# Kernel optimization log

Measured on AMD Instinct MI355X. Metric: run time of the kernel, lower is better.

The kernel has to match this reference:

```python
import jax, jax.numpy as jnp
import numpy as np

EPS = 1e-5  # torch BatchNorm default eps
SLOPE = 0.2  # LeakyReLU negative slope


def bn_apply(h, p):
    # p: (4, C) stacked [gamma, beta, running_mean, running_var]; h channel-last
    g, b, m, v = p[0], p[1], p[2], p[3]
    return (h - m) * (g * jax.lax.rsqrt(v + EPS)) + b


def graph_feature(x, k):
    # x: (B, N, C) -> (B, N, k, 2C) = concat(neighbor - center, center)
    inner = jnp.einsum('bnc,bmc->bnm', x, x)
    sq = jnp.sum(x * x, axis=-1)
    # negative squared pairwise distance (B, N, N)
    pd = 2.0 * inner - sq[:, :, None] - sq[:, None, :]
    idx = jax.lax.top_k(pd, k)[1]  # (B, N, k)
    nbr = jax.vmap(lambda xb, ib: xb[ib])(x, idx)  # (B, N, k, C) gather
    ctr = jnp.broadcast_to(x[:, :, None, :], nbr.shape)
    return jnp.concatenate([nbr - ctr, ctr], axis=-1)


def edge_block(h, w, bnp, k):
    # h: (B, N, C); w: (O, 2C) 1x1 conv weight; returns (B, N, O) after max over k
    f = graph_feature(h, k)
    z = jnp.einsum('bnkc,oc->bnko', f, w)
    z = jax.nn.leaky_relu(bn_apply(z, bnp), SLOPE)
    return jnp.max(z, axis=2)


def setup_inputs() -> dict:
    key = jax.random.key(0)
    ks = jax.random.split(key, 10)
    B, N, K = 16, 1024, 20
    emb, ncls = 1024, 40

    def bnp(c):
        return jnp.stack([jnp.ones(c), jnp.zeros(c), jnp.zeros(c), jnp.ones(c)])

    s = 0.05
    return {
        'x': jax.random.normal(ks[0], (B, 3, N), dtype=jnp.float32),
        'w1': jax.random.normal(ks[1], (64, 6), dtype=jnp.float32) * s,
        'bn1': bnp(64),
        'w2': jax.random.normal(ks[2], (64, 128), dtype=jnp.float32) * s,
        'bn2': bnp(64),
        'w3': jax.random.normal(ks[3], (128, 128), dtype=jnp.float32) * s,
        'bn3': bnp(128),
        'w4': jax.random.normal(ks[4], (256, 256), dtype=jnp.float32) * s,
        'bn4': bnp(256),
        'w5': jax.random.normal(ks[5], (emb, 512), dtype=jnp.float32) * s,
        'bn5': bnp(emb),
        'wl1': jax.random.normal(ks[6], (512, 2 * emb), dtype=jnp.float32) * s,
        'bn6': bnp(512),
        'wl2': jax.random.normal(ks[7], (256, 512), dtype=jnp.float32) * s,
        'bn7': bnp(256),
        'wl3': jax.random.normal(ks[8], (ncls, 256), dtype=jnp.float32) * s,
        'bl3': jax.random.normal(ks[9], (ncls,), dtype=jnp.float32) * s,
        'k': K,
    }


def reference(x, w1, bn1, w2, bn2, w3, bn3, w4, bn4, w5, bn5,
              wl1, bn6, wl2, bn7, wl3, bl3, k):
    # x: (B, 3, N) -> logits (B, num_classes); eval-mode BN, dropout = identity
    h0 = jnp.transpose(x, (0, 2, 1))  # (B, N, 3)
    x1 = edge_block(h0, w1, bn1, k)   # (B, N, 64)
    x2 = edge_block(x1, w2, bn2, k)   # (B, N, 64)
    x3 = edge_block(x2, w3, bn3, k)   # (B, N, 128)
    x4 = edge_block(x3, w4, bn4, k)   # (B, N, 256)
    h = jnp.concatenate([x1, x2, x3, x4], axis=-1)  # (B, N, 512)
    h = jax.nn.leaky_relu(bn_apply(jnp.einsum('bnc,oc->bno', h, w5), bn5), SLOPE)
    p = jnp.concatenate([jnp.max(h, axis=1), jnp.mean(h, axis=1)], axis=-1)  # (B, 2*emb)
    h = jax.nn.leaky_relu(bn_apply(p @ wl1.T, bn6), SLOPE)
    h = jax.nn.leaky_relu(bn_apply(h @ wl2.T, bn7), SLOPE)
    return h @ wl3.T + bl3
```

## Files before the change

### kernel.cpp

```cpp
#include <hip/hip_runtime.h>

#define BB 16
#define NN 1024
#define KNN 20
#define BNEPS 1e-5f

typedef __attribute__((ext_vector_type(8))) short short8;
typedef __attribute__((ext_vector_type(4))) float f32x4;

__device__ __forceinline__ float4 ld4(const float* p){ return *(const float4*)p; }
__device__ __forceinline__ void fma4(float4& a, float s, float4 w){
  a.x = fmaf(s, w.x, a.x); a.y = fmaf(s, w.y, a.y);
  a.z = fmaf(s, w.z, a.z); a.w = fmaf(s, w.w, a.w);
}
__device__ __forceinline__ void max4(float4& a, float4 v){
  a.x = fmaxf(a.x, v.x); a.y = fmaxf(a.y, v.y);
  a.z = fmaxf(a.z, v.z); a.w = fmaxf(a.w, v.w);
}
__device__ __forceinline__ unsigned short f2bf(float f){
  unsigned int u = __float_as_uint(f);
  u = (u + 0x7FFF + ((u >> 16) & 1)) >> 16;
  return (unsigned short)u;
}
__device__ __forceinline__ float bf2f(unsigned short u){
  return __uint_as_float(((unsigned int)u) << 16);
}
__device__ __forceinline__ f32x4 mfma16(short8 a, short8 b, f32x4 c){
  return __builtin_amdgcn_mfma_f32_16x16x32_bf16(a, b, c, 0, 0, 0);
}

__device__ __forceinline__ void top3_build(const float* rp, int kmr,
                                           float& a0, float& a1, float& a2,
                                           int& i0, int& i1, int& i2){
  a0 = -1e30f; a1 = -1e30f; a2 = -1e30f; i0 = 0; i1 = 0; i2 = 0;
#pragma unroll
  for (int r = 0; r < 4; r++){
    float4 t = ld4(rp + r*4);
    float tv[4] = {t.x, t.y, t.z, t.w};
#pragma unroll
    for (int q = 0; q < 4; q++){
      int e = r*4 + q;
      float v = ((kmr >> e) & 1) ? -1e30f : tv[q];
      bool b0 = v > a0, b1 = v > a1, b2 = v > a2;
      a2 = b1 ? a1 : (b2 ? v : a2); i2 = b1 ? i1 : (b2 ? e : i2);
      a1 = b0 ? a0 : (b1 ? v : a1); i1 = b0 ? i0 : (b1 ? e : i1);
      a0 = b0 ? v  : a0;            i0 = b0 ? e : i0;
    }
  }
}

__device__ __forceinline__ void topk_body(int bid, int tidx,
                                          const float* __restrict__ pd, int* __restrict__ idxOut){
  int w = tidx >> 6, lane = tidx & 63;
  const int xcd = bid & 7, j = bid >> 3;
  const int b = xcd + ((j >> 7) << 3);
  const int local = j & 127;
  int bn0 = (b*128 + local)*8 + w*2;
  const float* row0 = pd + (size_t)bn0*NN + lane*16;
  const float* row1 = row0 + NN;

  float c0v[2], c1v[2], c2v[2];
  int   c0i[2], c1i[2], c2i[2];
  int   km[2] = {0, 0};
  top3_build(row0, 0, c0v[0], c1v[0], c2v[0], c0i[0], c1i[0], c2i[0]);
  top3_build(row1, 0, c0v[1], c1v[1], c2v[1], c0i[1], c1i[1], c2i[1]);

  int* out0 = idxOut + (size_t)bn0*KNN;
  int* out1 = out0 + KNN;
  for (int it = 0; it < KNN; it++){
    float g0 = c0v[0], g1 = c0v[1];
#pragma unroll
    for (int s = 1; s < 64; s <<= 1){
      g0 = fmaxf(g0, __shfl_xor(g0, s));
      g1 = fmaxf(g1, __shfl_xor(g1, s));
    }
    int o0 = __ffsll(__ballot(c0v[0] == g0)) - 1;
    int o1 = __ffsll(__ballot(c0v[1] == g1)) - 1;
    bool u0 = (lane == o0), u1 = (lane == o1);
    if (u0) out0[it] = lane*16 + c0i[0];
    if (u1) out1[it] = lane*16 + c0i[1];
    km[0] |= u0 ? (1 << c0i[0]) : 0;
    km[1] |= u1 ? (1 << c0i[1]) : 0;
    c0v[0] = u0 ? c1v[0] : c0v[0];  c0i[0] = u0 ? c1i[0] : c0i[0];
    c1v[0] = u0 ? c2v[0] : c1v[0];  c1i[0] = u0 ? c2i[0] : c1i[0];
    c2v[0] = u0 ? -1e30f : c2v[0];
    c0v[1] = u1 ? c1v[1] : c0v[1];  c0i[1] = u1 ? c1i[1] : c0i[1];
    c1v[1] = u1 ? c2v[1] : c1v[1];  c1i[1] = u1 ? c2i[1] : c1i[1];
    c2v[1] = u1 ? -1e30f : c2v[1];
    if (it < KNN-1){
      bool rp0 = (c0v[0] == -1e30f) && (km[0] != 0xFFFF);
      bool rp1 = (c0v[1] == -1e30f) && (km[1] != 0xFFFF);
      if (__ballot(rp0 || rp1)){
        if (rp0) top3_build(row0, km[0], c0v[0], c1v[0], c2v[0], c0i[0], c1i[0], c2i[0]);
        if (rp1) top3_build(row1, km[1], c0v[1], c1v[1], c2v[1], c0i[1], c1i[1], c2i[1]);
      }
    }
  }
}

__device__ __forceinline__ void prep_w_dev(int i, const float* w, const float* bnp,
                                           float* wlT, float* dT, float* bias, int Cin, int Cpad, int Cout){
  if (i >= Cpad*Cout) return;
  int c = i / Cout, o = i - c*Cout;
  float s = bnp[o] * rsqrtf(bnp[3*Cout+o] + BNEPS);
  float wl = (c < Cin) ? w[(size_t)o*2*Cin + c] : 0.f;
  float wr = (c < Cin) ? w[(size_t)o*2*Cin + Cin + c] : 0.f;
  wlT[i] = wl * s;
  dT[i]  = (wr - wl) * s;
  if (c == 0) bias[o] = bnp[Cout+o] - bnp[2*Cout+o]*s;
}
__device__ __forceinline__ void prep_wbf_dev(int i, const float* w, const float* bnp,
                                             unsigned short* wlB, unsigned short* dB, float* bias,
                                             int Cin, int Cout){
  if (i >= Cin*Cout) return;
  int o = i / Cin, c = i - o*Cin;
  float s = bnp[o] * rsqrtf(bnp[3*Cout+o] + BNEPS);
  float wl = w[(size_t)o*2*Cin + c] * s;
  float wr = w[(size_t)o*2*Cin + Cin + c] * s;
  wlB[i] = f2bf(wl);
  dB[i]  = f2bf(wr - wl);
  if (c == 0) bias[o] = bnp[Cout+o] - bnp[2*Cout+o]*s;
}

__global__ __launch_bounds__(256) void k_init(const float* __restrict__ x, float* __restrict__ xt,
                                              unsigned short* __restrict__ hlo, float* __restrict__ sq,
                                              const float* __restrict__ w1, const float* __restrict__ bn1,
                                              const float* __restrict__ w2, const float* __restrict__ bn2,
                                              const float* __restrict__ w3, const float* __restrict__ bn3,
                                              const float* __restrict__ w4, const float* __restrict__ bn4,
                                              const float* __restrict__ w5, const float* __restrict__ bn5,
                                              float* __restrict__ wlT1, float* __restrict__ dT1, float* __restrict__ bias1,
                                              unsigned short* __restrict__ wlB2, unsigned short* __restrict__ dB2, float* __restrict__ bias2,
                                              unsigned short* __restrict__ wlB3, unsigned short* __restrict__ dB3, float* __restrict__ bias3,
                                              unsigned short* __restrict__ wlB4, unsigned short* __restrict__ dB4, float* __restrict__ bias4,
                                              unsigned short* __restrict__ w5b, float* __restrict__ b5){
  const int t = threadIdx.x;
  if (blockIdx.x < 64){
    int i = blockIdx.x*256 + t;
    int b = i >> 10, n = i & 1023;
    const float* xb = x + (size_t)b*3*NN;
    float4 v;
    v.x = xb[0*NN+n]; v.y = xb[1*NN+n]; v.z = xb[2*NN+n]; v.w = 0.f;
    ((float4*)xt)[i] = v;
    unsigned short hx = f2bf(v.x), hy = f2bf(v.y), hz = f2bf(v.z);
    float rx = v.x - bf2f(hx), ry = v.y - bf2f(hy), rz = v.z - bf2f(hz);
    unsigned short lx = f2bf(rx), ly = f2bf(ry), lz = f2bf(rz);
    float ex = bf2f(hx)+bf2f(lx), ey = bf2f(hy)+bf2f(ly), ez = bf2f(hz)+bf2f(lz);
    sq[i] = ex*ex + ey*ey + ez*ez;
    ushort4 h4 = {hx, hy, hz, 0};
    ushort4 l4 = {lx, ly, lz, 0};
    ushort4 z4 = {0, 0, 0, 0};
    unsigned short* pa = hlo + (size_t)i*512 + 256;
    unsigned short* pb = hlo + (size_t)i*512 + 288;
    *(ushort4*)(pa+0) = h4; *(ushort4*)(pa+4) = l4; *(ushort4*)(pa+8) = h4;
    *(ushort4*)(pb+0) = h4; *(ushort4*)(pb+4) = h4; *(ushort4*)(pb+8) = l4;
#pragma unroll
    for (int s = 12; s < 32; s += 4){ *(ushort4*)(pa+s) = z4; *(ushort4*)(pb+s) = z4; }
    return;
  }
  int bid = blockIdx.x - 64;
  if (bid < 1){
    prep_w_dev(t, w1, bn1, wlT1, dT1, bias1, 3, 4, 64);
  } else if (bid < 17){
    prep_wbf_dev((bid-1)*256 + t, w2, bn2, wlB2, dB2, bias2, 64, 64);
  } else if (bid < 49){
    prep_wbf_dev((bid-17)*256 + t, w3, bn3, wlB3, dB3, bias3, 64, 128);
  } else if (bid < 177){
    prep_wbf_dev((bid-49)*256 + t, w4, bn4, wlB4, dB4, bias4, 128, 256);
  } else {
    int i = (bid-177)*256 + t;
    int o = i >> 9, c = i & 511;
    float s = bn5[o] * rsqrtf(bn5[3*1024+o] + BNEPS);
    w5b[i] = f2bf(w5[(size_t)o*512 + c] * s);
    if (c == 0) b5[o] = bn5[1024+o] - bn5[2*1024+o]*s;
  }
}

template<int CC>
__global__ __launch_bounds__(256) void k_pdm(const unsigned short* __restrict__ hbi,
                                             const unsigned short* __restrict__ hlo,
                                             const float* __restrict__ sq,
                                             float* __restrict__ pd){
  __shared__ char sm[20480];
  char* As = sm; char* Bs = sm + 10240;
  const int tid = threadIdx.x, lane = tid & 63, w = tid >> 6;
  const int l15 = lane & 15, quad = lane >> 4;
  const int bid = blockIdx.x;
  const int xcd = bid & 7, j = bid >> 3;
  const int b = xcd + ((j >> 6) << 3);
  const int rt = (j >> 3) & 7, ct = j & 7;
  const size_t ar0 = (size_t)b*NN + rt*128;
  const size_t br0 = (size_t)b*NN + ct*128;
  const int colb = ct*128;

  f32x4 acc[2][8];
  f32x4 zero = {0.f,0.f,0.f,0.f};
#pragma unroll
  for (int i = 0; i < 2; i++)
#pragma unroll
    for (int j2 = 0; j2 < 8; j2++) acc[i][j2] = zero;

  for (int k0 = 0; k0 < 3*CC; k0 += 32){
    int seg = k0 / CC, off = k0 - seg*CC;
    const unsigned short* Ap = (seg == 1) ? hlo : hbi;
    const unsigned short* Bp = (seg == 2) ? hlo : hbi;
#pragma unroll
    for (int i = 0; i < 2; i++){
      int e = tid + i*256;
      int r = e >> 2, sg = e & 3;
      *(float4*)(As + r*80 + sg*16) = *(const float4*)(Ap + (ar0+r)*512 + off + sg*8);
      *(float4*)(Bs + r*80 + sg*16) = *(const float4*)(Bp + (br0+r)*512 + off + sg*8);
    }
    __syncthreads();
    short8 af0 = *(short8*)(As + (w*32 + l15)*80 + quad*16);
    short8 af1 = *(short8*)(As + (w*32 + 16 + l15)*80 + quad*16);
#pragma unroll
    for (int ns = 0; ns < 8; ns++){
      short8 bf = *(short8*)(Bs + (ns*16 + l15)*80 + quad*16);
      acc[0][ns] = mfma16(af0, bf, acc[0][ns]);
      acc[1][ns] = mfma16(af1, bf, acc[1][ns]);
    }
    __syncthreads();
  }

  float* L = (float*)sm;
#pragma unroll
  for (int p = 0; p < 4; p++){
    const int ms = p >> 1, nh = p & 1;
    __syncthreads();
#pragma unroll
    for (int ns = 0; ns < 4; ns++){
      f32x4 a = acc[ms][nh*4 + ns];
      float sqv = sq[br0 + (nh*4+ns)*16 + l15];
#pragma unroll
      for (int r = 0; r < 4; r++)
        L[(w*16 + quad*4 + r)*68 + ns*16 + l15] = 2.f*a[r] - sqv;
    }
    __syncthreads();
#pragma unroll
    for (int k = 0; k < 4; k++){
      int e = tid + k*256;
      int lr = e >> 4, c4 = (e & 15)*4;
      int grow = (int)ar0 + (lr >> 4)*32 + ms*16 + (lr & 15);
      *(float4*)(pd + (size_t)grow*NN + colb + nh*64 + c4) = *(float4*)(L + lr*68 + c4);
    }
  }
}

__global__ __launch_bounds__(256) void k_pdm1(const unsigned short* __restrict__ hlo,
                                              const float* __restrict__ sq,
                                              float* __restrict__ pd){
  __shared__ char sm[20480];
  char* As = sm; char* Bs = sm + 10240;
  const int tid = threadIdx.x, lane = tid & 63, w = tid >> 6;
  const int l15 = lane & 15, quad = lane >> 4;
  const int bid = blockIdx.x;
  const int xcd = bid & 7, j = bid >> 3;
  const int b = xcd + ((j >> 6) << 3);
  const int rt = (j >> 3) & 7, ct = j & 7;
  const size_t ar0 = (size_t)b*NN + rt*128;
  const size_t br0 = (size_t)b*NN + ct*128;
  const int colb = ct*128;

#pragma unroll
  for (int i = 0; i < 2; i++){
    int e = tid + i*256;
    int r = e >> 2, sg = e & 3;
    *(float4*)(As + r*80 + sg*16) = *(const float4*)(hlo + (ar0+r)*512 + 256 + sg*8);
    *(float4*)(Bs + r*80 + sg*16) = *(const float4*)(hlo + (br0+r)*512 + 288 + sg*8);
  }
  __syncthreads();

  f32x4 acc[2][8];
  f32x4 zero = {0.f,0.f,0.f,0.f};
#pragma unroll
  for (int i = 0; i < 2; i++)
#pragma unroll
    for (int j2 = 0; j2 < 8; j2++) acc[i][j2] = zero;

  short8 af0 = *(short8*)(As + (w*32 + l15)*80 + quad*16);
  short8 af1 = *(short8*)(As + (w*32 + 16 + l15)*80 + quad*16);
#pragma unroll
  for (int ns = 0; ns < 8; ns++){
    short8 bf = *(short8*)(Bs + (ns*16 + l15)*80 + quad*16);
    acc[0][ns] = mfma16(af0, bf, acc[0][ns]);
    acc[1][ns] = mfma16(af1, bf, acc[1][ns]);
  }

  float* L = (float*)sm;
#pragma unroll
  for (int p = 0; p < 4; p++){
    const int ms = p >> 1, nh = p & 1;
    __syncthreads();
#pragma unroll
    for (int ns = 0; ns < 4; ns++){
      f32x4 a = acc[ms][nh*4 + ns];
      float sqv = sq[br0 + (nh*4+ns)*16 + l15];
#pragma unroll
      for (int r = 0; r < 4; r++)
        L[(w*16 + quad*4 + r)*68 + ns*16 + l15] = 2.f*a[r] - sqv;
    }
    __syncthreads();
#pragma unroll
    for (int k = 0; k < 4; k++){
      int e = tid + k*256;
      int lr = e >> 4, c4 = (e & 15)*4;
      int grow = (int)ar0 + (lr >> 4)*32 + ms*16 + (lr & 15);
      *(float4*)(pd + (size_t)grow*NN + colb + nh*64 + c4) = *(float4*)(L + lr*68 + c4);
    }
  }
}

template<int K, int NY>
__global__ __launch_bounds__(256) void k_tkuv(const float* __restrict__ pd, int* __restrict__ idxOut,
                                              const unsigned short* __restrict__ hbi,
                                              const unsigned short* __restrict__ wB,
                                              float* __restrict__ Z, int ldz){
  __shared__ char sm[20480];
  if (blockIdx.x < 2048){
    topk_body(blockIdx.x, threadIdx.x, pd, idxOut);
    return;
  }
  char* As = sm; char* Bs = sm + 10240;
  const int tid = threadIdx.x, lane = tid & 63, w = tid >> 6;
  const int l15 = lane & 15, quad = lane >> 4;
  const int jj = blockIdx.x - 2048;
  const int bx = jj & 127;
  const int t = ((bx & 7) << 3) | ((bx >> 3) & 7) | (bx & 64);
  const int n0 = (jj >> 7)*128, r0 = t*128;

  f32x4 acc[2][8];
  f32x4 zero = {0.f,0.f,0.f,0.f};
#pragma unroll
  for (int i = 0; i < 2; i++)
#pragma unroll
    for (int j = 0; j < 8; j++) acc[i][j] = zero;

  for (int k0 = 0; k0 < K; k0 += 32){
#pragma unroll
    for (int i = 0; i < 2; i++){
      int e = tid + i*256;
      int r = e >> 2, sg = e & 3;
      *(float4*)(As + r*80 + sg*16) = *(const float4*)(hbi + ((size_t)(r0+r))*512 + k0 + sg*8);
      *(float4*)(Bs + r*80 + sg*16) = *(const float4*)(wB  + ((size_t)(n0+r))*K   + k0 + sg*8);
    }
    __syncthreads();
    short8 af0 = *(short8*)(As + (w*32 + l15)*80 + quad*16);
    short8 af1 = *(short8*)(As + (w*32 + 16 + l15)*80 + quad*16);
#pragma unroll
    for (int ns = 0; ns < 8; ns++){
      short8 bf = *(short8*)(Bs + (ns*16 + l15)*80 + quad*16);
      acc[0][ns] = mfma16(af0, bf, acc[0][ns]);
      acc[1][ns] = mfma16(af1, bf, acc[1][ns]);
    }
    __syncthreads();
  }

#pragma unroll
  for (int ms = 0; ms < 2; ms++){
#pragma unroll
    for (int ns = 0; ns < 8; ns++){
      f32x4 a = acc[ms][ns];
      int row = r0 + w*32 + ms*16 + quad*4;
      int col = n0 + ns*16 + l15;
#pragma unroll
      for (int r = 0; r < 4; r++)
        Z[(size_t)(row+r)*ldz + col] = a[r];
    }
  }
}

__global__ __launch_bounds__(256) void k_tkuv1(const float* __restrict__ pd, int* __restrict__ idxOut,
                                               const float* __restrict__ xt,
                                               const float* __restrict__ wlT, const float* __restrict__ dT,
                                               float* __restrict__ Z){
  if (blockIdx.x < 2048){
    topk_body(blockIdx.x, threadIdx.x, pd, idxOut);
    return;
  }
  const int bid = blockIdx.x - 2048;
  const int pb = ((bid >> 10) << 10) | ((bid & 7) << 7) | ((bid >> 3) & 127);
  int t = pb*256 + threadIdx.x;
  int n = t >> 5, q = t & 31;
  float4 xv = ld4(xt + (size_t)n*4);
  const float* wp = (q < 16) ? (wlT + q*4) : (dT + (q-16)*4);
  float4 a = make_float4(0.f,0.f,0.f,0.f);
  fma4(a, xv.x, ld4(wp + 0*64));
  fma4(a, xv.y, ld4(wp + 1*64));
  fma4(a, xv.z, ld4(wp + 2*64));
  fma4(a, xv.w, ld4(wp + 3*64));
  *(float4*)(Z + (size_t)n*128 + q*4) = a;
}

template<int COUT, int P, bool WLO>
__global__ __launch_bounds__(256) void k_gmax(const float* __restrict__ Z,
                                              const float* __restrict__ bias,
                                              const int* __restrict__ knn_idx,
                                              unsigned short* __restrict__ hbo,
                                              unsigned short* __restrict__ hloo,
                                              float* __restrict__ sqo){
  constexpr int QPP = COUT/4;
  constexpr int BPB = 1024/P;
  constexpr int SHF = (P == 16) ? 6 : (P == 8) ? 7 : 8;
  __shared__ int idxS[P*KNN];
  const int tid = threadIdx.x;
  const int bid = blockIdx.x;
  const int pb = ((bid >> (SHF+3)) << (SHF+3)) | ((bid & 7) << SHF) | ((bid >> 3) & (BPB-1));
  const int p0 = pb * P;
  for (int t = tid; t < P*KNN; t += 256) idxS[t] = knn_idx[(size_t)p0*KNN + t];
  __syncthreads();

  const int p = tid / QPP, q = tid - p*QPP;
  const int base = p0 & ~1023;
  const int ldz = 2*COUT;
  const float* Zq = Z + q*4;

  float4 m = make_float4(-1e30f,-1e30f,-1e30f,-1e30f);
#pragma unroll
  for (int j = 0; j < KNN; j++){
    int mr = idxS[p*KNN + j];
    max4(m, ld4(Zq + (size_t)(base + mr)*ldz));
  }
  float4 ctr = ld4(Z + (size_t)(p0+p)*ldz + COUT + q*4);
  float4 bs  = ld4(bias + q*4);
  float4 y;
  y.x = m.x + ctr.x + bs.x; y.x = fmaxf(y.x, 0.2f*y.x);
  y.y = m.y + ctr.y + bs.y; y.y = fmaxf(y.y, 0.2f*y.y);
  y.z = m.z + ctr.z + bs.z; y.z = fmaxf(y.z, 0.2f*y.z);
  y.w = m.w + ctr.w + bs.w; y.w = fmaxf(y.w, 0.2f*y.w);

  size_t pi = (size_t)(p0 + p);
  ushort4 hv; hv.x = f2bf(y.x); hv.y = f2bf(y.y); hv.z = f2bf(y.z); hv.w = f2bf(y.w);
  *(ushort4*)(hbo + pi*512 + q*4) = hv;
  if (WLO){
    ushort4 lv;
    lv.x = f2bf(y.x - bf2f(hv.x)); lv.y = f2bf(y.y - bf2f(hv.y));
    lv.z = f2bf(y.z - bf2f(hv.z)); lv.w = f2bf(y.w - bf2f(hv.w));
    *(ushort4*)(hloo + pi*512 + q*4) = lv;
    float ex = bf2f(hv.x)+bf2f(lv.x), ey = bf2f(hv.y)+bf2f(lv.y);
    float ez = bf2f(hv.z)+bf2f(lv.z), ew = bf2f(hv.w)+bf2f(lv.w);
    float s4 = ex*ex + ey*ey + ez*ez + ew*ew;
#pragma unroll
    for (int sh = 1; sh < QPP; sh <<= 1) s4 += __shfl_xor(s4, sh);
    if (q == 0) sqo[pi] = s4;
  }
}

__global__ __launch_bounds__(256) void k_conv5m(const unsigned short* __restrict__ hb,
                                                const unsigned short* __restrict__ w5b,
                                                const float* __restrict__ b5,
                                                float* __restrict__ pmax, float* __restrict__ psum){
  __shared__ char sm[20480 + 4096];
  char* As = sm; char* Bs = sm + 10240;
  float* red = (float*)(sm + 20480);
  const int tid = threadIdx.x, lane = tid & 63, w = tid >> 6;
  const int l15 = lane & 15, quad = lane >> 4;
  const int n0 = blockIdx.y*128, r0 = blockIdx.x*128;

  f32x4 acc[2][8];
  f32x4 zero = {0.f,0.f,0.f,0.f};
#pragma unroll
  for (int i = 0; i < 2; i++)
#pragma unroll
    for (int j = 0; j < 8; j++) acc[i][j] = zero;

  for (int k0 = 0; k0 < 512; k0 += 32){
#pragma unroll
    for (int i = 0; i < 2; i++){
      int e = tid + i*256;
      int r = e >> 2, sg = e & 3;
      *(float4*)(As + r*80 + sg*16) = *(const float4*)(hb  + ((size_t)(r0+r))*512 + k0 + sg*8);
      *(float4*)(Bs + r*80 + sg*16) = *(const float4*)(w5b + ((size_t)(n0+r))*512 + k0 + sg*8);
    }
    __syncthreads();
    short8 af0 = *(short8*)(As + (w*32 + l15)*80 + quad*16);
    short8 af1 = *(short8*)(As + (w*32 + 16 + l15)*80 + quad*16);
#pragma unroll
    for (int ns = 0; ns < 8; ns++){
      short8 bf = *(short8*)(Bs + (ns*16 + l15)*80 + quad*16);
      acc[0][ns] = mfma16(af0, bf, acc[0][ns]);
      acc[1][ns] = mfma16(af1, bf, acc[1][ns]);
    }
    __syncthreads();
  }

#pragma unroll
  for (int ns = 0; ns < 8; ns++){
    float bv = b5[n0 + ns*16 + l15];
    float mx = -1e30f, sum = 0.f;
#pragma unroll
    for (int ms = 0; ms < 2; ms++){
      float* a = (float*)&acc[ms][ns];
#pragma unroll
      for (int r = 0; r < 4; r++){
        float v = a[r] + bv; v = fmaxf(v, 0.2f*v);
        mx = fmaxf(mx, v); sum += v;
      }
    }
    for (int s = 16; s < 64; s <<= 1){
      mx = fmaxf(mx, __shfl_xor(mx, s));
      sum += __shfl_xor(sum, s);
    }
    if (quad == 0){ red[(w*8 + ns)*16 + l15] = mx; red[512 + (w*8 + ns)*16 + l15] = sum; }
  }
  __syncthreads();
  if (tid < 128){
    int ns = tid >> 4, ci = tid & 15;
    float mx = -1e30f, sum = 0.f;
#pragma unroll
    for (int w2 = 0; w2 < 4; w2++){
      mx = fmaxf(mx, red[(w2*8 + ns)*16 + ci]);
      sum += red[512 + (w2*8 + ns)*16 + ci];
    }
    pmax[(size_t)blockIdx.x*1024 + n0 + tid] = mx;
    psum[(size_t)blockIdx.x*1024 + n0 + tid] = sum;
  }
}

__global__ __launch_bounds__(256) void k_fc1(const float* __restrict__ pmax, const float* __restrict__ psum,
                                             const float* __restrict__ wl1, const float* __restrict__ bn6,
                                             float* __restrict__ h1){
  __shared__ float pS[2048];
  const int b = blockIdx.y, t = threadIdx.x;
  for (int f = t; f < 512; f += 256){
    float4 r;
    if (f < 256){
      r = ld4(pmax + (size_t)(b*8)*1024 + f*4);
#pragma unroll
      for (int ch = 1; ch < 8; ch++) max4(r, ld4(pmax + (size_t)(b*8+ch)*1024 + f*4));
    } else {
      int o = (f-256)*4;
      r = ld4(psum + (size_t)(b*8)*1024 + o);
#pragma unroll
      for (int ch = 1; ch < 8; ch++){
        float4 s = ld4(psum + (size_t)(b*8+ch)*1024 + o);
        r.x += s.x; r.y += s.y; r.z += s.z; r.w += s.w;
      }
      r.x *= (1.f/1024.f); r.y *= (1.f/1024.f); r.z *= (1.f/1024.f); r.w *= (1.f/1024.f);
    }
    ((float4*)pS)[f] = r;
  }
  __syncthreads();
  const int ol = t >> 4, ch = t & 15;
  const int o = blockIdx.x*16 + ol;
  const float* wr = wl1 + (size_t)o*2048;
  float acc = 0.f;
#pragma unroll
  for (int j = 0; j < 32; j++){
    int c = ch*4 + j*64;
    float4 wv = ld4(wr + c);
    acc += pS[c]*wv.x + pS[c+1]*wv.y + pS[c+2]*wv.z + pS[c+3]*wv.w;
  }
#pragma unroll
  for (int s = 1; s < 16; s <<= 1) acc += __shfl_xor(acc, s);
  if (ch == 0){
    float s = bn6[o] * rsqrtf(bn6[3*512+o] + BNEPS);
    float y = (acc - bn6[2*512+o])*s + bn6[512+o];
    h1[(size_t)b*512 + o] = fmaxf(y, 0.2f*y);
  }
}

__global__ __launch_bounds__(256) void k_fc2(const float* __restrict__ h1,
                                             const float* __restrict__ wl2, const float* __restrict__ bn7,
                                             float* __restrict__ h2){
  __shared__ float hS[512];
  const int b = blockIdx.y, t = threadIdx.x;
  if (t < 128) ((float4*)hS)[t] = ((const float4*)(h1 + (size_t)b*512))[t];
  __syncthreads();
  const int ol = t >> 4, ch = t & 15;
  const int o = blockIdx.x*16 + ol;
  const float* wr = wl2 + (size_t)o*512;
  float acc = 0.f;
#pragma unroll
  for (int j = 0; j < 8; j++){
    int c = ch*4 + j*64;
    float4 wv = ld4(wr + c);
    acc += hS[c]*wv.x + hS[c+1]*wv.y + hS[c+2]*wv.z + hS[c+3]*wv.w;
  }
#pragma unroll
  for (int s = 1; s < 16; s <<= 1) acc += __shfl_xor(acc, s);
  if (ch == 0){
    float s = bn7[o] * rsqrtf(bn7[3*256+o] + BNEPS);
    float y = (acc - bn7[2*256+o])*s + bn7[256+o];
    h2[(size_t)b*256 + o] = fmaxf(y, 0.2f*y);
  }
}

__global__ __launch_bounds__(64) void k_fc3(const float* __restrict__ h2,
                                            const float* __restrict__ wl3, const float* __restrict__ bl3,
                                            float* __restrict__ out){
  const int o = blockIdx.x, b = blockIdx.y, lane = threadIdx.x;
  float4 wv = ld4(wl3 + (size_t)o*256 + lane*4);
  float4 hv = ld4(h2 + (size_t)b*256 + lane*4);
  float acc = hv.x*wv.x + hv.y*wv.y + hv.z*wv.z + hv.w*wv.w;
#pragma unroll
  for (int s = 1; s < 64; s <<= 1) acc += __shfl_xor(acc, s);
  if (lane == 0) out[(size_t)b*40 + o] = acc + bl3[o];
}

extern "C" void kernel_launch(void* const* d_in, const int* in_sizes, int n_in,
                              void* d_out, int out_size, void* d_ws, size_t ws_size,
                              hipStream_t stream) {
  (void)in_sizes; (void)n_in; (void)out_size; (void)ws_size;
  const float* x   = (const float*)d_in[0];
  const float* w1  = (const float*)d_in[1];
  const float* bn1 = (const float*)d_in[2];
  const float* w2  = (const float*)d_in[3];
  const float* bn2 = (const float*)d_in[4];
  const float* w3  = (const float*)d_in[5];
  const float* bn3 = (const float*)d_in[6];
  const float* w4  = (const float*)d_in[7];
  const float* bn4 = (const float*)d_in[8];
  const float* w5  = (const float*)d_in[9];
  const float* bn5 = (const float*)d_in[10];
  const float* wl1 = (const float*)d_in[11];
  const float* bn6 = (const float*)d_in[12];
  const float* wl2 = (const float*)d_in[13];
  const float* bn7 = (const float*)d_in[14];
  const float* wl3 = (const float*)d_in[15];
  const float* bl3 = (const float*)d_in[16];
  float* out = (float*)d_out;

  float* ws    = (float*)d_ws;
  float* xt    = ws;
  float* sqb   = xt + 65536;
  int*   idxb  = (int*)(sqb + 16384);
  float* pd    = (float*)(idxb + 327680);
  unsigned short* hlo = (unsigned short*)(pd + 16777216);
  float* wlT1  = (float*)(hlo + 8388608);
  float* dT1   = wlT1 + 256;
  float* bias1 = dT1 + 256;
  float* bias2 = bias1 + 64;
  float* bias3 = bias2 + 64;
  float* bias4 = bias3 + 128;
  float* b5    = bias4 + 256;
  float* pmax  = b5 + 1024;
  float* psum  = pmax + 131072;
  float* pool  = psum + 131072;
  float* h1b   = pool + 32768;
  float* h2b   = h1b + 8192;
  unsigned short* hb   = (unsigned short*)(h2b + 4096);
  unsigned short* wlB2 = hb + (size_t)16384*512;
  unsigned short* dB2  = wlB2 + 4096;
  unsigned short* wlB3 = dB2 + 4096;
  unsigned short* dB3  = wlB3 + 8192;
  unsigned short* wlB4 = dB3 + 8192;
  unsigned short* dB4  = wlB4 + 32768;
  unsigned short* w5b  = dB4 + 32768;
  float* Z = (float*)(w5b + 524288);

  k_init<<<2289, 256, 0, stream>>>(x, xt, hlo, sqb,
                                   w1, bn1, w2, bn2, w3, bn3, w4, bn4, w5, bn5,
                                   wlT1, dT1, bias1, wlB2, dB2, bias2,
                                   wlB3, dB3, bias3, wlB4, dB4, bias4, w5b, b5);

  k_pdm1<<<1024, 256, 0, stream>>>(hlo, sqb, pd);
  k_tkuv1<<<4096, 256, 0, stream>>>(pd, idxb, xt, wlT1, dT1, Z);
  k_gmax<64,16,true><<<1024, 256, 0, stream>>>(Z, bias1, idxb, hb, hlo, sqb);

  k_pdm<64><<<1024, 256, 0, stream>>>(hb, hlo, sqb, pd);
  k_tkuv<64,1><<<2048+128, 256, 0, stream>>>(pd, idxb, hb, wlB2, Z, 128);
  k_gmax<64,16,true><<<1024, 256, 0, stream>>>(Z, bias2, idxb, hb + 64, hlo + 64, sqb);

  k_pdm<64><<<1024, 256, 0, stream>>>(hb + 64, hlo + 64, sqb, pd);
  k_tkuv<64,2><<<2048+256, 256, 0, stream>>>(pd, idxb, hb + 64, wlB3, Z, 256);
  k_gmax<128,8,true><<<2048, 256, 0, stream>>>(Z, bias3, idxb, hb + 128, hlo + 128, sqb);

  k_pdm<128><<<1024, 256, 0, stream>>>(hb + 128, hlo + 128, sqb, pd);
  k_tkuv<128,4><<<2048+512, 256, 0, stream>>>(pd, idxb, hb + 128, wlB4, Z, 512);
  k_gmax<256,4,false><<<4096, 256, 0, stream>>>(Z, bias4, idxb, hb + 256, nullptr, nullptr);

  k_conv5m<<<dim3(128,8), 256, 0, stream>>>(hb, w5b, b5, pmax, psum);
  k_fc1<<<dim3(32,16), 256, 0, stream>>>(pmax, psum, wl1, bn6, h1b);
  k_fc2<<<dim3(16,16), 256, 0, stream>>>(h1b, wl2, bn7, h2b);
  k_fc3<<<dim3(40,16), 64, 0, stream>>>(h2b, wl3, bl3, out);
}
```

Baseline: 403.4 us.

## Split edge-conv stages by batch halves and fuse across layers to overlap

Each edge-conv layer's pairwise-distance, top-k, projection and gather-max stages now run on two halves of the batch. They are fused into skewed combined kernels (D1/D2/D3), so one half's stage runs alongside the other half's different stage in the same launch. The intent is to mix compute-bound GEMM blocks with memory- and latency-bound top-k and gather blocks, shrinking tail effects and idle gaps between dependent launches. The Z buffer uses a fixed row stride of 512 so both halves can share it. The cost is more complex indexing, extra kernel variants, and possible cache contention between the mixed workloads.

Measured after the change: 439.6 us. 9.0% more time.

```diff
diff --git a/kernel.cpp b/kernel.cpp
--- a/kernel.cpp
+++ b/kernel.cpp
@@ -4,6 +4,7 @@
 #define NN 1024
 #define KNN 20
 #define BNEPS 1e-5f
+#define LDZ 512
 
 typedef __attribute__((ext_vector_type(8))) short short8;
 typedef __attribute__((ext_vector_type(4))) float f32x4;
@@ -49,12 +50,9 @@
   }
 }
 
-__device__ __forceinline__ void topk_body(int bid, int tidx,
+__device__ __forceinline__ void topk_rows(int b, int local, int tidx,
                                           const float* __restrict__ pd, int* __restrict__ idxOut){
   int w = tidx >> 6, lane = tidx & 63;
-  const int xcd = bid & 7, j = bid >> 3;
-  const int b = xcd + ((j >> 7) << 3);
-  const int local = j & 127;
   int bn0 = (b*128 + local)*8 + w*2;
   const float* row0 = pd + (size_t)bn0*NN + lane*16;
   const float* row1 = row0 + NN;
@@ -96,6 +94,13 @@
       }
     }
   }
+}
+__device__ __forceinline__ void topk_full(int bid, int tidx, const float* pd, int* idxOut){
+  const int xcd = bid & 7, j = bid >> 3;
+  topk_rows(xcd + ((j >> 7) << 3), j & 127, tidx, pd, idxOut);
+}
+__device__ __forceinline__ void topk_half(int bid, int b0, int tidx, const float* pd, int* idxOut){
+  topk_rows((bid & 7) + b0, (bid >> 3) & 127, tidx, pd, idxOut);
 }
 
 __device__ __forceinline__ void prep_w_dev(int i, const float* w, const float* bnp,
@@ -177,17 +182,16 @@
 }
 
 template<int CC>
-__global__ __launch_bounds__(256) void k_pdm(const unsigned short* __restrict__ hbi,
-                                             const unsigned short* __restrict__ hlo,
-                                             const float* __restrict__ sq,
-                                             float* __restrict__ pd){
-  __shared__ char sm[20480];
+__device__ __forceinline__ void pdm_body(char* sm, int bid, int b0,
+                                         const unsigned short* __restrict__ hbi,
+                                         const unsigned short* __restrict__ hlo,
+                                         const float* __restrict__ sq,
+                                         float* __restrict__ pd){
   char* As = sm; char* Bs = sm + 10240;
   const int tid = threadIdx.x, lane = tid & 63, w = tid >> 6;
   const int l15 = lane & 15, quad = lane >> 4;
-  const int bid = blockIdx.x;
-  const int xcd = bid & 7, j = bid >> 3;
-  const int b = xcd + ((j >> 6) << 3);
+  const int b = (bid & 7) + b0;
+  const int j = bid >> 3;
   const int rt = (j >> 3) & 7, ct = j & 7;
   const size_t ar0 = (size_t)b*NN + rt*128;
   const size_t br0 = (size_t)b*NN + ct*128;
@@ -311,23 +315,17 @@
   }
 }
 
-template<int K, int NY>
-__global__ __launch_bounds__(256) void k_tkuv(const float* __restrict__ pd, int* __restrict__ idxOut,
-                                              const unsigned short* __restrict__ hbi,
-                                              const unsigned short* __restrict__ wB,
-                                              float* __restrict__ Z, int ldz){
-  __shared__ char sm[20480];
-  if (blockIdx.x < 2048){
-    topk_body(blockIdx.x, threadIdx.x, pd, idxOut);
-    return;
-  }
+template<int K>
+__device__ __forceinline__ void uv_body(char* sm, int bid, int b0,
+                                        const unsigned short* __restrict__ hbi,
+                                        const unsigned short* __restrict__ wB,
+                                        float* __restrict__ Z){
   char* As = sm; char* Bs = sm + 10240;
   const int tid = threadIdx.x, lane = tid & 63, w = tid >> 6;
   const int l15 = lane & 15, quad = lane >> 4;
-  const int jj = blockIdx.x - 2048;
-  const int bx = jj & 127;
-  const int t = ((bx & 7) << 3) | ((bx >> 3) & 7) | (bx & 64);
-  const int n0 = (jj >> 7)*128, r0 = t*128;
+  const int bx = bid & 63, ny = bid >> 6;
+  const int t8 = ((bx & 7) << 3) | ((bx >> 3) & 7);
+  const int n0 = ny*128, r0 = (t8 + b0*8)*128;
 
   f32x4 acc[2][8];
   f32x4 zero = {0.f,0.f,0.f,0.f};
@@ -365,8 +363,60 @@
       int col = n0 + ns*16 + l15;
 #pragma unroll
       for (int r = 0; r < 4; r++)
-        Z[(size_t)(row+r)*ldz + col] = a[r];
-    }
+        Z[(size_t)(row+r)*LDZ + col] = a[r];
+    }
+  }
+}
+
+template<int COUT, int P, bool WLO>
+__device__ __forceinline__ void gmax_body(char* smraw, int bid, int b0,
+                                          const float* __restrict__ Z,
+                                          const float* __restrict__ bias,
+                                          const int* __restrict__ knn_idx,
+                                          unsigned short* __restrict__ hbo,
+                                          unsigned short* __restrict__ hloo,
+                                          float* __restrict__ sqo){
+  constexpr int QPP = COUT/4;
+  constexpr int BPB = 1024/P;
+  int* idxS = (int*)smraw;
+  const int tid = threadIdx.x;
+  const int pb = ((bid & 7) + b0)*BPB + ((bid >> 3) & (BPB-1));
+  const int p0 = pb * P;
+  for (int t = tid; t < P*KNN; t += 256) idxS[t] = knn_idx[(size_t)p0*KNN + t];
+  __syncthreads();
+
+  const int p = tid / QPP, q = tid - p*QPP;
+  const int base = p0 & ~1023;
+  const float* Zq = Z + q*4;
+
+  float4 m = make_float4(-1e30f,-1e30f,-1e30f,-1e30f);
+#pragma unroll
+  for (int j = 0; j < KNN; j++){
+    int mr = idxS[p*KNN + j];
+    max4(m, ld4(Zq + (size_t)(base + mr)*LDZ));
+  }
+  float4 ctr = ld4(Z + (size_t)(p0+p)*LDZ + COUT + q*4);
+  float4 bs  = ld4(bias + q*4);
+  float4 y;
+  y.x = m.x + ctr.x + bs.x; y.x = fmaxf(y.x, 0.2f*y.x);
+  y.y = m.y + ctr.y + bs.y; y.y = fmaxf(y.y, 0.2f*y.y);
+  y.z = m.z + ctr.z + bs.z; y.z = fmaxf(y.z, 0.2f*y.z);
+  y.w = m.w + ctr.w + bs.w; y.w = fmaxf(y.w, 0.2f*y.w);
+
+  size_t pi = (size_t)(p0 + p);
+  ushort4 hv; hv.x = f2bf(y.x); hv.y = f2bf(y.y); hv.z = f2bf(y.z); hv.w = f2bf(y.w);
+  *(ushort4*)(hbo + pi*512 + q*4) = hv;
+  if (WLO){
+    ushort4 lv;
+    lv.x = f2bf(y.x - bf2f(hv.x)); lv.y = f2bf(y.y - bf2f(hv.y));
+    lv.z = f2bf(y.z - bf2f(hv.z)); lv.w = f2bf(y.w - bf2f(hv.w));
+    *(ushort4*)(hloo + pi*512 + q*4) = lv;
+    float ex = bf2f(hv.x)+bf2f(lv.x), ey = bf2f(hv.y)+bf2f(lv.y);
+    float ez = bf2f(hv.z)+bf2f(lv.z), ew = bf2f(hv.w)+bf2f(lv.w);
+    float s4 = ex*ex + ey*ey + ez*ez + ew*ew;
+#pragma unroll
+    for (int sh = 1; sh < QPP; sh <<= 1) s4 += __shfl_xor(s4, sh);
+    if (q == 0) sqo[pi] = s4;
   }
 }
 
@@ -375,7 +425,7 @@
                                                const float* __restrict__ wlT, const float* __restrict__ dT,
                                                float* __restrict__ Z){
   if (blockIdx.x < 2048){
-    topk_body(blockIdx.x, threadIdx.x, pd, idxOut);
+    topk_full(blockIdx.x, threadIdx.x, pd, idxOut);
     return;
   }
   const int bid = blockIdx.x - 2048;
@@ -389,61 +439,55 @@
   fma4(a, xv.y, ld4(wp + 1*64));
   fma4(a, xv.z, ld4(wp + 2*64));
   fma4(a, xv.w, ld4(wp + 3*64));
-  *(float4*)(Z + (size_t)n*128 + q*4) = a;
+  *(float4*)(Z + (size_t)n*LDZ + q*4) = a;
 }
 
 template<int COUT, int P, bool WLO>
-__global__ __launch_bounds__(256) void k_gmax(const float* __restrict__ Z,
-                                              const float* __restrict__ bias,
-                                              const int* __restrict__ knn_idx,
-                                              unsigned short* __restrict__ hbo,
-                                              unsigned short* __restrict__ hloo,
-                                              float* __restrict__ sqo){
-  constexpr int QPP = COUT/4;
-  constexpr int BPB = 1024/P;
-  constexpr int SHF = (P == 16) ? 6 : (P == 8) ? 7 : 8;
-  __shared__ int idxS[P*KNN];
-  const int tid = threadIdx.x;
-  const int bid = blockIdx.x;
-  const int pb = ((bid >> (SHF+3)) << (SHF+3)) | ((bid & 7) << SHF) | ((bid >> 3) & (BPB-1));
-  const int p0 = pb * P;
-  for (int t = tid; t < P*KNN; t += 256) idxS[t] = knn_idx[(size_t)p0*KNN + t];
-  __syncthreads();
-
-  const int p = tid / QPP, q = tid - p*QPP;
-  const int base = p0 & ~1023;
-  const int ldz = 2*COUT;
-  const float* Zq = Z + q*4;
-
-  float4 m = make_float4(-1e30f,-1e30f,-1e30f,-1e30f);
-#pragma unroll
-  for (int j = 0; j < KNN; j++){
-    int mr = idxS[p*KNN + j];
-    max4(m, ld4(Zq + (size_t)(base + mr)*ldz));
-  }
-  float4 ctr = ld4(Z + (size_t)(p0+p)*ldz + COUT + q*4);
-  float4 bs  = ld4(bias + q*4);
-  float4 y;
-  y.x = m.x + ctr.x + bs.x; y.x = fmaxf(y.x, 0.2f*y.x);
-  y.y = m.y + ctr.y + bs.y; y.y = fmaxf(y.y, 0.2f*y.y);
-  y.z = m.z + ctr.z + bs.z; y.z = fmaxf(y.z, 0.2f*y.z);
-  y.w = m.w + ctr.w + bs.w; y.w = fmaxf(y.w, 0.2f*y.w);
-
-  size_t pi = (size_t)(p0 + p);
-  ushort4 hv; hv.x = f2bf(y.x); hv.y = f2bf(y.y); hv.z = f2bf(y.z); hv.w = f2bf(y.w);
-  *(ushort4*)(hbo + pi*512 + q*4) = hv;
-  if (WLO){
-    ushort4 lv;
-    lv.x = f2bf(y.x - bf2f(hv.x)); lv.y = f2bf(y.y - bf2f(hv.y));
-    lv.z = f2bf(y.z - bf2f(hv.z)); lv.w = f2bf(y.w - bf2f(hv.w));
-    *(ushort4*)(hloo + pi*512 + q*4) = lv;
-    float ex = bf2f(hv.x)+bf2f(lv.x), ey = bf2f(hv.y)+bf2f(lv.y);
-    float ez = bf2f(hv.z)+bf2f(lv.z), ew = bf2f(hv.w)+bf2f(lv.w);
-    float s4 = ex*ex + ey*ey + ez*ez + ew*ew;
-#pragma unroll
-    for (int sh = 1; sh < QPP; sh <<= 1) s4 += __shfl_xor(s4, sh);
-    if (q == 0) sqo[pi] = s4;
-  }
+__global__ __launch_bounds__(256) void k_gmaxH(int b0, const float* __restrict__ Z,
+                                               const float* __restrict__ bias, const int* __restrict__ idx,
+                                               unsigned short* __restrict__ hbo,
+                                               unsigned short* __restrict__ hloo, float* __restrict__ sqo){
+  __shared__ char sm[20480];
+  gmax_body<COUT,P,WLO>(sm, blockIdx.x, b0, Z, bias, idx, hbo, hloo, sqo);
+}
+
+template<int CC, int COUT, int P, bool WLO>
+__global__ __launch_bounds__(256) void k_D1(const unsigned short* __restrict__ hbi,
+                                            const unsigned short* __restrict__ hloi,
+                                            const float* __restrict__ sq, float* __restrict__ pd,
+                                            const float* __restrict__ Z, const float* __restrict__ bias,
+                                            const int* __restrict__ idx,
+                                            unsigned short* __restrict__ hbo,
+                                            unsigned short* __restrict__ hloo, float* __restrict__ sqo){
+  __shared__ char sm[20480];
+  if (blockIdx.x < 512) pdm_body<CC>(sm, blockIdx.x, 0, hbi, hloi, sq, pd);
+  else gmax_body<COUT,P,WLO>(sm, blockIdx.x - 512, 8, Z, bias, idx, hbo, hloo, sqo);
+}
+
+template<int CC, int K, int NY>
+__global__ __launch_bounds__(256) void k_D2(const unsigned short* __restrict__ hbi,
+                                            const unsigned short* __restrict__ hloi,
+                                            const float* __restrict__ sq, float* __restrict__ pd,
+                                            const unsigned short* __restrict__ wB,
+                                            float* __restrict__ Z, int* __restrict__ idxOut){
+  __shared__ char sm[20480];
+  if (blockIdx.x < 512) pdm_body<CC>(sm, blockIdx.x, 8, hbi, hloi, sq, pd);
+  else if (blockIdx.x < 512 + NY*64) uv_body<K>(sm, blockIdx.x - 512, 0, hbi, wB, Z);
+  else topk_half(blockIdx.x - (512 + NY*64), 0, threadIdx.x, pd, idxOut);
+}
+
+template<int K, int NY, int COUT, int P, bool WLO>
+__global__ __launch_bounds__(256) void k_D3(const float* __restrict__ pd, int* __restrict__ idxOut,
+                                            const unsigned short* __restrict__ hbi,
+                                            const unsigned short* __restrict__ wB, float* __restrict__ Z,
+                                            const float* __restrict__ bias,
+                                            unsigned short* __restrict__ hbo,
+                                            unsigned short* __restrict__ hloo, float* __restrict__ sqo){
+  __shared__ char sm[20480];
+  constexpr int GH = 8 * (1024/P);
+  if (blockIdx.x < GH) gmax_body<COUT,P,WLO>(sm, blockIdx.x, 0, Z, bias, idxOut, hbo, hloo, sqo);
+  else if (blockIdx.x < GH + NY*64) uv_body<K>(sm, blockIdx.x - GH, 8, hbi, wB, Z);
+  else topk_half(blockIdx.x - (GH + NY*64), 8, threadIdx.x, pd, idxOut);
 }
 
 __global__ __launch_bounds__(256) void k_conv5m(const unsigned short* __restrict__ hb,
@@ -656,19 +700,20 @@
 
   k_pdm1<<<1024, 256, 0, stream>>>(hlo, sqb, pd);
   k_tkuv1<<<4096, 256, 0, stream>>>(pd, idxb, xt, wlT1, dT1, Z);
-  k_gmax<64,16,true><<<1024, 256, 0, stream>>>(Z, bias1, idxb, hb, hlo, sqb);
-
-  k_pdm<64><<<1024, 256, 0, stream>>>(hb, hlo, sqb, pd);
-  k_tkuv<64,1><<<2048+128, 256, 0, stream>>>(pd, idxb, hb, wlB2, Z, 128);
-  k_gmax<64,16,true><<<1024, 256, 0, stream>>>(Z, bias2, idxb, hb + 64, hlo + 64, sqb);
-
-  k_pdm<64><<<1024, 256, 0, stream>>>(hb + 64, hlo + 64, sqb, pd);
-  k_tkuv<64,2><<<2048+256, 256, 0, stream>>>(pd, idxb, hb + 64, wlB3, Z, 256);
-  k_gmax<128,8,true><<<2048, 256, 0, stream>>>(Z, bias3, idxb, hb + 128, hlo + 128, sqb);
-
-  k_pdm<128><<<1024, 256, 0, stream>>>(hb + 128, hlo + 128, sqb, pd);
-  k_tkuv<128,4><<<2048+512, 256, 0, stream>>>(pd, idxb, hb + 128, wlB4, Z, 512);
-  k_gmax<256,4,false><<<4096, 256, 0, stream>>>(Z, bias4, idxb, hb + 256, nullptr, nullptr);
+  k_gmaxH<64,16,true><<<512, 256, 0, stream>>>(0, Z, bias1, idxb, hb, hlo, sqb);
+
+  k_D1<64,64,16,true><<<1024, 256, 0, stream>>>(hb, hlo, sqb, pd, Z, bias1, idxb, hb, hlo, sqb);
+  k_D2<64,64,1><<<1600, 256, 0, stream>>>(hb, hlo, sqb, pd, wlB2, Z, idxb);
+  k_D3<64,1,64,16,true><<<1600, 256, 0, stream>>>(pd, idxb, hb, wlB2, Z, bias2, hb+64, hlo+64, sqb);
+
+  k_D1<64,64,16,true><<<1024, 256, 0, stream>>>(hb+64, hlo+64, sqb, pd, Z, bias2, idxb, hb+64, hlo+64, sqb);
+  k_D2<64,64,2><<<1664, 256, 0, stream>>>(hb+64, hlo+64, sqb, pd, wlB3, Z, idxb);
+  k_D3<64,2,128,8,true><<<2176, 256, 0, stream>>>(pd, idxb, hb+64, wlB3, Z, bias3, hb+128, hlo+128, sqb);
+
+  k_D1<128,128,8,true><<<1536, 256, 0, stream>>>(hb+128, hlo+128, sqb, pd, Z, bias3, idxb, hb+128, hlo+128, sqb);
+  k_D2<128,128,4><<<1792, 256, 0, stream>>>(hb+128, hlo+128, sqb, pd, wlB4, Z, idxb);
+  k_D3<128,4,256,4,false><<<3328, 256, 0, stream>>>(pd, idxb, hb+128, wlB4, Z, bias4, hb+256, nullptr, nullptr);
+  k_gmaxH<256,4,false><<<2048, 256, 0, stream>>>(8, Z, bias4, idxb, hb+256, nullptr, nullptr);
 
   k_conv5m<<<dim3(128,8), 256, 0, stream>>>(hb, w5b, b5, pmax, psum);
   k_fc1<<<dim3(32,16), 256, 0, stream>>>(pmax, psum, wl1, bn6, h1b);
```
